# Optimization experiments

Hardware: AMD Instinct MI355X
Metric: run time of the kernel (lower is better)

The kernel has to match this reference:

```python
import jax, jax.numpy as jnp
import numpy as np

# irreps layout: 64x0e + 64x1o + 64x2e  ->  flattened dim = 64*(1+3+5) = 576
MULS = (64, 64, 64)
DIMS = (1, 3, 5)   # 2l+1 for l = 0, 1, 2
N = 262144


def setup_inputs() -> dict:
    key = jax.random.key(0)
    k0, k1, k2, k3 = jax.random.split(key, 4)
    total = sum(m * d for m, d in zip(MULS, DIMS))  # 576
    x = jax.random.normal(k0, (N, total), dtype=jnp.float32)
    # FunctionalLinear weights: one [mul_in, mul_out] matrix per (irrep_in, irrep_out) path.
    # With gradient_normalization='path', init std = sqrt(alpha)^(1-1) = 1.
    w0 = jax.random.normal(k1, (64, 64), dtype=jnp.float32)
    w1 = jax.random.normal(k2, (64, 64), dtype=jnp.float32)
    w2 = jax.random.normal(k3, (64, 64), dtype=jnp.float32)
    return {"x": x, "w0": w0, "w1": w1, "w2": w2}


def reference(x, w0, w1, w2):
    # e3nn Linear with irreps_in == irreps_out == 64x0e+64x1o+64x2e:
    # per irrep l: out[:, w, i] = sqrt(1/mul_in) * sum_u x[:, u, i] * W[u, w]
    # (path_normalization='element' -> alpha = 1/mul_in; gradient_normalization='path'
    #  -> full sqrt(alpha) applied in the forward pass.)
    ws = (w0, w1, w2)
    outs = []
    off = 0
    for mul, d, w in zip(MULS, DIMS, ws):
        xl = x[..., off:off + mul * d].reshape(x.shape[:-1] + (mul, d))  # [N, mul, 2l+1]
        off += mul * d
        scale = jnp.sqrt(jnp.asarray(1.0 / mul, dtype=x.dtype))
        yl = scale * jnp.einsum('nui,uw->nwi', xl, w)  # small per-irrep matmul
        outs.append(yl.reshape(x.shape[:-1] + (mul * d,)))
    return jnp.concatenate(outs, axis=-1)  # [N, 576]
```

## Files before the change

### kernel.cpp

```cpp
#include <hip/hip_runtime.h>


typedef _Float16 half4  __attribute__((ext_vector_type(4)));
typedef float    f32x4  __attribute__((ext_vector_type(4)));

#define RPB      16
#define NROWS    262144
#define ROWF     576
#define HTROWS   8
#define LDS_BYTES (HTROWS * ROWF * 4)

template<int D, int OFF, int SEGROW, int F4PR>
__device__ __forceinline__ void stage_seg(unsigned char* lds, const float* __restrict__ xrow0, int tid) {
#pragma unroll
  for (int it = 0; it < RPB * F4PR / 256; ++it) {
    int t = tid + it * 256;
    int row = t / F4PR;
    int f4  = t - row * F4PR;
    f32x4 v = *(const f32x4*)(xrow0 + (long long)row * ROWF + OFF + f4 * 4);
    int idx = f4 * 4;
    if (D == 1) {
      int lrow = SEGROW + row;
      int b = (lrow * 128 + idx * 2) ^ ((lrow & 7) << 4);
      half4 h = { (_Float16)v[0], (_Float16)v[1], (_Float16)v[2], (_Float16)v[3] };
      *(half4*)(lds + b) = h;
    } else {
#pragma unroll
      for (int j = 0; j < 4; ++j) {
        int u = (idx + j) / D;
        int i = (idx + j) - u * D;
        int lrow = SEGROW + row * D + i;
        int b = (lrow * 128 + u * 2) ^ ((lrow & 7) << 4);
        *(_Float16*)(lds + b) = (_Float16)v[j];
      }
    }
  }
}

__device__ __forceinline__ void load_bfrag(const float* __restrict__ W, int wt,
                                           int lane15, int laneq, half4 bf[4]) {
  int w = wt * 16 + lane15;
#pragma unroll
  for (int s = 0; s < 4; ++s) {
    int u0 = s * 16 + laneq * 4;
#pragma unroll
    for (int j = 0; j < 4; ++j)
      bf[s][j] = (_Float16)W[(u0 + j) * 64 + w];
  }
}

template<int SEGROW, int MT>
__device__ __forceinline__ void compute_seg(const unsigned char* lds, int lane15, int laneq,
                                            const half4 bf[4], f32x4 acc[MT]) {
  const int coff = laneq * 8;
#pragma unroll
  for (int mt = 0; mt < MT; ++mt) {
    int arow  = SEGROW + mt * 16 + lane15;
    int abase = arow * 128;
    int aswz  = (arow & 7) << 4;
    acc[mt] = (f32x4){0.f, 0.f, 0.f, 0.f};
#pragma unroll
    for (int s = 0; s < 4; ++s) {
      half4 a = *(const half4*)(lds + abase + ((s * 32 + coff) ^ aswz));
      acc[mt] = __builtin_amdgcn_mfma_f32_16x16x16f16(a, bf[s], acc[mt], 0, 0, 0);
    }
  }
}

template<int D, int OFF, int MT, int PHASE>
__device__ __forceinline__ void scatter_seg(unsigned char* lds, int wt, int lane15, int laneq,
                                            const f32x4 acc[MT]) {
  const int w = wt * 16 + lane15;
#pragma unroll
  for (int mt = 0; mt < MT; ++mt) {
#pragma unroll
    for (int j = 0; j < 4; ++j) {
      int r = mt * 16 + laneq * 4 + j;
      int n = r / D;
      int i = r - n * D;
      bool sel = PHASE ? (n >= HTROWS) : (n < HTROWS);
      if (sel)
        *(float*)(lds + (n - PHASE * HTROWS) * (ROWF * 4) + (OFF + w * D + i) * 4)
            = 0.125f * acc[mt][j];
    }
  }
}

__device__ __forceinline__ void copy_half(const unsigned char* lds, float* __restrict__ dst, int tid) {
#pragma unroll
  for (int k = 0; k < 4; ++k) {
    int q = tid + k * 256;
    *(f32x4*)(dst + q * 4) = *(const f32x4*)(lds + q * 16);
  }
  if (tid < 128) {
    int q = tid + 1024;
    *(f32x4*)(dst + q * 4) = *(const f32x4*)(lds + q * 16);
  }
}

__global__ __launch_bounds__(256, 8) void linear_irreps(
    const float* __restrict__ x,
    const float* __restrict__ w0, const float* __restrict__ w1, const float* __restrict__ w2,
    float* __restrict__ out) {
  __shared__ __align__(16) unsigned char lds[LDS_BYTES];
  const int tid = threadIdx.x;
  const int lane = tid & 63, wave = tid >> 6;
  const int lane15 = lane & 15, laneq = lane >> 4;
  const int wt = wave;
  const long long base = (long long)blockIdx.x * (RPB * ROWF);

  half4 bf0[4], bf1[4], bf2[4];
  load_bfrag(w0, wt, lane15, laneq, bf0);
  load_bfrag(w1, wt, lane15, laneq, bf1);
  load_bfrag(w2, wt, lane15, laneq, bf2);

  stage_seg<1,   0,   0, 16>(lds, x + base, tid);
  stage_seg<3,  64,  16, 48>(lds, x + base, tid);
  stage_seg<5, 256,  64, 80>(lds, x + base, tid);
  __syncthreads();

  f32x4 acc1[1], acc3[3], acc5[5];
  compute_seg<  0, 1>(lds, lane15, laneq, bf0, acc1);
  compute_seg< 16, 3>(lds, lane15, laneq, bf1, acc3);
  compute_seg< 64, 5>(lds, lane15, laneq, bf2, acc5);
  __syncthreads();

  scatter_seg<1,   0, 1, 0>(lds, wt, lane15, laneq, acc1);
  scatter_seg<3,  64, 3, 0>(lds, wt, lane15, laneq, acc3);
  scatter_seg<5, 256, 5, 0>(lds, wt, lane15, laneq, acc5);
  __syncthreads();
  copy_half(lds, out + base, tid);
  __syncthreads();

  scatter_seg<1,   0, 1, 1>(lds, wt, lane15, laneq, acc1);
  scatter_seg<3,  64, 3, 1>(lds, wt, lane15, laneq, acc3);
  scatter_seg<5, 256, 5, 1>(lds, wt, lane15, laneq, acc5);
  __syncthreads();
  copy_half(lds, out + base + HTROWS * ROWF, tid);
}

extern "C" void kernel_launch(void* const* d_in, const int* in_sizes, int n_in,
                              void* d_out, int out_size, void* d_ws, size_t ws_size,
                              hipStream_t stream) {
  const float* x  = (const float*)d_in[0];
  const float* w0 = (const float*)d_in[1];
  const float* w1 = (const float*)d_in[2];
  const float* w2 = (const float*)d_in[3];
  float* out = (float*)d_out;
  linear_irreps<<<NROWS / RPB, 256, 0, stream>>>(x, w0, w1, w2, out);
}
```

Before: 260.6 us.

## Make kernel persistent with producer/consumer waves and double-buffered input staging

Launches a fixed 2048 workgroups of 512 threads, each looping over several 16-row tiles. Four producer waves stage the next tile into a second LDS buffer while four consumer waves run the MFMAs and scatter results for the current tile. The aim is to overlap global loads with compute and the output copy, and to cut per-block launch and weight-fragment loading overhead. In exchange, fewer waves per CU issue loads, LDS use per workgroup grows, and every tile now needs four block-wide barriers, which may lower memory-level parallelism.

Result: faster. 249.2 us (-4.4%).

```diff
diff --git a/kernel.cpp b/kernel.cpp
--- a/kernel.cpp
+++ b/kernel.cpp
@@ -4,14 +4,19 @@
 typedef _Float16 half4  __attribute__((ext_vector_type(4)));
 typedef float    f32x4  __attribute__((ext_vector_type(4)));
 
-#define RPB      16
-#define NROWS    262144
-#define ROWF     576
-#define HTROWS   8
-#define LDS_BYTES (HTROWS * ROWF * 4)
+#define NROWS   262144
+#define ROWF    576
+#define RPB     16
+#define TILEF   (RPB * ROWF)
+#define NTILES  (NROWS / RPB)
+#define NWG     2048
+#define TPW     (NTILES / NWG)
+#define STG_B   18432
+#define HT_B    18432
+#define LDS_B   (2 * STG_B + HT_B)
 
 template<int D, int OFF, int SEGROW, int F4PR>
-__device__ __forceinline__ void stage_seg(unsigned char* lds, const float* __restrict__ xrow0, int tid) {
+__device__ __forceinline__ void stage_seg(unsigned char* stg, const float* __restrict__ xrow0, int tid) {
 #pragma unroll
   for (int it = 0; it < RPB * F4PR / 256; ++it) {
     int t = tid + it * 256;
@@ -23,7 +28,7 @@
       int lrow = SEGROW + row;
       int b = (lrow * 128 + idx * 2) ^ ((lrow & 7) << 4);
       half4 h = { (_Float16)v[0], (_Float16)v[1], (_Float16)v[2], (_Float16)v[3] };
-      *(half4*)(lds + b) = h;
+      *(half4*)(stg + b) = h;
     } else {
 #pragma unroll
       for (int j = 0; j < 4; ++j) {
@@ -31,10 +36,16 @@
         int i = (idx + j) - u * D;
         int lrow = SEGROW + row * D + i;
         int b = (lrow * 128 + u * 2) ^ ((lrow & 7) << 4);
-        *(_Float16*)(lds + b) = (_Float16)v[j];
+        *(_Float16*)(stg + b) = (_Float16)v[j];
       }
     }
   }
+}
+
+__device__ __forceinline__ void stage_tile(unsigned char* stg, const float* __restrict__ xs, int tid) {
+  stage_seg<1,   0,  0, 16>(stg, xs, tid);
+  stage_seg<3,  64, 16, 48>(stg, xs, tid);
+  stage_seg<5, 256, 64, 80>(stg, xs, tid);
 }
 
 __device__ __forceinline__ void load_bfrag(const float* __restrict__ W, int wt,
@@ -50,7 +61,7 @@
 }
 
 template<int SEGROW, int MT>
-__device__ __forceinline__ void compute_seg(const unsigned char* lds, int lane15, int laneq,
+__device__ __forceinline__ void compute_seg(const unsigned char* stg, int lane15, int laneq,
                                             const half4 bf[4], f32x4 acc[MT]) {
   const int coff = laneq * 8;
 #pragma unroll
@@ -61,14 +72,14 @@
     acc[mt] = (f32x4){0.f, 0.f, 0.f, 0.f};
 #pragma unroll
     for (int s = 0; s < 4; ++s) {
-      half4 a = *(const half4*)(lds + abase + ((s * 32 + coff) ^ aswz));
+      half4 a = *(const half4*)(stg + abase + ((s * 32 + coff) ^ aswz));
       acc[mt] = __builtin_amdgcn_mfma_f32_16x16x16f16(a, bf[s], acc[mt], 0, 0, 0);
     }
   }
 }
 
 template<int D, int OFF, int MT, int PHASE>
-__device__ __forceinline__ void scatter_seg(unsigned char* lds, int wt, int lane15, int laneq,
+__device__ __forceinline__ void scatter_seg(unsigned char* outl, int wt, int lane15, int laneq,
                                             const f32x4 acc[MT]) {
   const int w = wt * 16 + lane15;
 #pragma unroll
@@ -78,65 +89,80 @@
       int r = mt * 16 + laneq * 4 + j;
       int n = r / D;
       int i = r - n * D;
-      bool sel = PHASE ? (n >= HTROWS) : (n < HTROWS);
+      bool sel = PHASE ? (n >= 8) : (n < 8);
       if (sel)
-        *(float*)(lds + (n - PHASE * HTROWS) * (ROWF * 4) + (OFF + w * D + i) * 4)
+        *(float*)(outl + (n - PHASE * 8) * (ROWF * 4) + (OFF + w * D + i) * 4)
             = 0.125f * acc[mt][j];
     }
   }
 }
 
-__device__ __forceinline__ void copy_half(const unsigned char* lds, float* __restrict__ dst, int tid) {
+__device__ __forceinline__ void copy_half(const unsigned char* outl, float* __restrict__ dst, int tid) {
 #pragma unroll
-  for (int k = 0; k < 4; ++k) {
-    int q = tid + k * 256;
-    *(f32x4*)(dst + q * 4) = *(const f32x4*)(lds + q * 16);
+  for (int k = 0; k < 2; ++k) {
+    int q = tid + k * 512;
+    *(f32x4*)(dst + q * 4) = *(const f32x4*)(outl + q * 16);
   }
   if (tid < 128) {
     int q = tid + 1024;
-    *(f32x4*)(dst + q * 4) = *(const f32x4*)(lds + q * 16);
+    *(f32x4*)(dst + q * 4) = *(const f32x4*)(outl + q * 16);
   }
 }
 
-__global__ __launch_bounds__(256, 8) void linear_irreps(
+__global__ __launch_bounds__(512, 2) void linear_irreps(
     const float* __restrict__ x,
     const float* __restrict__ w0, const float* __restrict__ w1, const float* __restrict__ w2,
     float* __restrict__ out) {
-  __shared__ __align__(16) unsigned char lds[LDS_BYTES];
+  __shared__ __align__(16) unsigned char lds[LDS_B];
+  unsigned char* outl = lds + 2 * STG_B;
   const int tid = threadIdx.x;
-  const int lane = tid & 63, wave = tid >> 6;
+  const int wave = tid >> 6, lane = tid & 63;
   const int lane15 = lane & 15, laneq = lane >> 4;
-  const int wt = wave;
-  const long long base = (long long)blockIdx.x * (RPB * ROWF);
+  const bool producer = (wave < 4);
+  const int wt = wave & 3;
 
   half4 bf0[4], bf1[4], bf2[4];
   load_bfrag(w0, wt, lane15, laneq, bf0);
   load_bfrag(w1, wt, lane15, laneq, bf1);
   load_bfrag(w2, wt, lane15, laneq, bf2);
 
-  stage_seg<1,   0,   0, 16>(lds, x + base, tid);
-  stage_seg<3,  64,  16, 48>(lds, x + base, tid);
-  stage_seg<5, 256,  64, 80>(lds, x + base, tid);
+  const long long t0 = (long long)blockIdx.x * TPW;
+
+  if (producer) stage_tile(lds, x + t0 * TILEF, tid);
   __syncthreads();
 
-  f32x4 acc1[1], acc3[3], acc5[5];
-  compute_seg<  0, 1>(lds, lane15, laneq, bf0, acc1);
-  compute_seg< 16, 3>(lds, lane15, laneq, bf1, acc3);
-  compute_seg< 64, 5>(lds, lane15, laneq, bf2, acc5);
-  __syncthreads();
+  for (int k = 0; k < TPW; ++k) {
+    const long long tt = t0 + k;
+    unsigned char* cur = lds + (k & 1) * STG_B;
+    unsigned char* nxt = lds + ((k & 1) ^ 1) * STG_B;
+    f32x4 acc1[1], acc3[3], acc5[5];
 
-  scatter_seg<1,   0, 1, 0>(lds, wt, lane15, laneq, acc1);
-  scatter_seg<3,  64, 3, 0>(lds, wt, lane15, laneq, acc3);
-  scatter_seg<5, 256, 5, 0>(lds, wt, lane15, laneq, acc5);
-  __syncthreads();
-  copy_half(lds, out + base, tid);
-  __syncthreads();
+    if (producer) {
+      if (k + 1 < TPW) stage_tile(nxt, x + (tt + 1) * TILEF, tid);
+    } else {
+      compute_seg< 0, 1>(cur, lane15, laneq, bf0, acc1);
+      compute_seg<16, 3>(cur, lane15, laneq, bf1, acc3);
+      compute_seg<64, 5>(cur, lane15, laneq, bf2, acc5);
+      scatter_seg<1,   0, 1, 0>(outl, wt, lane15, laneq, acc1);
+      scatter_seg<3,  64, 3, 0>(outl, wt, lane15, laneq, acc3);
+      scatter_seg<5, 256, 5, 0>(outl, wt, lane15, laneq, acc5);
+    }
+    __syncthreads();
 
-  scatter_seg<1,   0, 1, 1>(lds, wt, lane15, laneq, acc1);
-  scatter_seg<3,  64, 3, 1>(lds, wt, lane15, laneq, acc3);
-  scatter_seg<5, 256, 5, 1>(lds, wt, lane15, laneq, acc5);
-  __syncthreads();
-  copy_half(lds, out + base + HTROWS * ROWF, tid);
+    float* dst = out + tt * TILEF;
+    copy_half(outl, dst, tid);
+    __syncthreads();
+
+    if (!producer) {
+      scatter_seg<1,   0, 1, 1>(outl, wt, lane15, laneq, acc1);
+      scatter_seg<3,  64, 3, 1>(outl, wt, lane15, laneq, acc3);
+      scatter_seg<5, 256, 5, 1>(outl, wt, lane15, laneq, acc5);
+    }
+    __syncthreads();
+
+    copy_half(outl, dst + 8 * ROWF, tid);
+    __syncthreads();
+  }
 }
 
 extern "C" void kernel_launch(void* const* d_in, const int* in_sizes, int n_in,
@@ -147,5 +173,5 @@
   const float* w1 = (const float*)d_in[2];
   const float* w2 = (const float*)d_in[3];
   float* out = (float*)d_out;
-  linear_irreps<<<NROWS / RPB, 256, 0, stream>>>(x, w0, w1, w2, out);
+  linear_irreps<<<NWG, 512, 0, stream>>>(x, w0, w1, w2, out);
 }
```
